# Performance work log

Hardware: AMD Instinct MI355X
Metric: run time of the kernel (lower is better)

Reference implementation:

```python
import jax, jax.numpy as jnp
import numpy as np
import math

H = 16          # num_attention_heads
D = 64          # attention_head_size
MAX_POS = 1024  # max_position_embeddings


def setup_inputs() -> dict:
    key = jax.random.key(0)
    ks = jax.random.split(key, 6)
    B, S, HID = 4, 1024, 1024
    scale = 1.0 / math.sqrt(HID)
    return {
        "hidden_states": jax.random.normal(ks[0], (B, S, HID), jnp.float32),
        "attention_mask": jnp.zeros((B, 1, 1, S), jnp.float32),
        "Wq": jax.random.normal(ks[1], (HID, HID), jnp.float32) * scale,
        "bq": jnp.zeros((HID,), jnp.float32),
        "Wk": jax.random.normal(ks[2], (HID, HID), jnp.float32) * scale,
        "bk": jnp.zeros((HID,), jnp.float32),
        "Wv": jax.random.normal(ks[3], (HID, HID), jnp.float32) * scale,
        "bv": jnp.zeros((HID,), jnp.float32),
        "dist_emb": jax.random.normal(ks[4], (2 * MAX_POS - 1, D), jnp.float32) * 0.02,
    }


def _split_heads(x):
    # [B,S,H*D] -> [B,H,S,D]
    B, S, _ = x.shape
    return x.reshape(B, S, H, D).transpose(0, 2, 1, 3)


def reference(hidden_states, attention_mask, Wq, bq, Wk, bk, Wv, bv, dist_emb):
    B, S, _ = hidden_states.shape
    q = _split_heads(hidden_states @ Wq.T + bq)   # [B,H,S,D]
    k = _split_heads(hidden_states @ Wk.T + bk)
    v = _split_heads(hidden_states @ Wv.T + bv)

    scores = jnp.einsum("bhqd,bhkd->bhqk", q, k)  # [B,H,S,S]

    # relative_key_query positional bias
    pos_l = jnp.arange(S)[:, None]
    pos_r = jnp.arange(S)[None, :]
    distance = pos_l - pos_r + (MAX_POS - 1)      # [S,S] in [0, 2*MAX_POS-2]
    pos_emb = dist_emb[distance]                  # [S,S,D]
    rel_q = jnp.einsum("bhld,lrd->bhlr", q, pos_emb)
    rel_k = jnp.einsum("bhrd,lrd->bhlr", k, pos_emb)
    scores = (scores + rel_q + rel_k) / math.sqrt(D)

    scores = scores + attention_mask
    probs = jax.nn.softmax(scores, axis=-1)
    ctx = jnp.einsum("bhqk,bhkd->bhqd", probs, v)  # [B,H,S,D]
    ctx = ctx.transpose(0, 2, 1, 3).reshape(B, S, H * D)
    return ctx
```

## Files before the change

kernel.cpp:

```cpp
#include <hip/hip_runtime.h>
#include <hip/hip_bf16.h>

#define B_   4
#define S_   1024
#define HID_ 1024
#define H_   16
#define D_   64

typedef __attribute__((ext_vector_type(4))) float f32x4;
typedef __attribute__((ext_vector_type(8))) __bf16 bf16v8;
typedef __attribute__((ext_vector_type(8))) unsigned short u16x8;

#define MFMA16(a, b, c) __builtin_amdgcn_mfma_f32_16x16x32_bf16((a), (b), (c), 0, 0, 0)
#define GLOAD16(gp, lp)                                                              \
    __builtin_amdgcn_global_load_lds((const __attribute__((address_space(1))) void*)(gp), \
                                     (__attribute__((address_space(3))) void*)(lp), 16, 0, 0)

__device__ __forceinline__ unsigned short f2bs_hw(float f) {
    __bf16 h = (__bf16)f;
    return __builtin_bit_cast(unsigned short, h);
}
__device__ __forceinline__ unsigned pack2bf(float a, float b) {
    unsigned short lo = f2bs_hw(a), hi = f2bs_hw(b);
    return (unsigned)lo | ((unsigned)hi << 16);
}
__device__ __forceinline__ float bs2f(unsigned short s) {
    union { unsigned u; float f; } v; v.u = ((unsigned)s) << 16;
    return v.f;
}

__global__ void conv_kernel(const float* __restrict__ src, unsigned short* __restrict__ dst,
                            int n4) {
    int i = blockIdx.x * 256 + threadIdx.x;
    if (i < n4) {
        float4 x = *(const float4*)(src + (size_t)i * 4);
        uint2 o;
        o.x = pack2bf(x.x, x.y);
        o.y = pack2bf(x.z, x.w);
        *(uint2*)(dst + (size_t)i * 4) = o;
    }
}

__global__ void conv4_kernel(const float* __restrict__ Wq, const float* __restrict__ Wk,
                             const float* __restrict__ Wv, const float* __restrict__ E,
                             unsigned short* __restrict__ Wqb, unsigned short* __restrict__ Wkb,
                             unsigned short* __restrict__ Wvb, unsigned short* __restrict__ Eb) {
    int bid = blockIdx.x;
    const float* src;
    unsigned short* dst;
    int n4, base;
    if (bid < 1024)      { src = Wq; dst = Wqb; n4 = 262144; base = bid; }
    else if (bid < 2048) { src = Wk; dst = Wkb; n4 = 262144; base = bid - 1024; }
    else if (bid < 3072) { src = Wv; dst = Wvb; n4 = 262144; base = bid - 2048; }
    else                 { src = E;  dst = Eb;  n4 = 32752;  base = bid - 3072; }
    int i = base * 256 + threadIdx.x;
    if (i < n4) {
        float4 x = *(const float4*)(src + (size_t)i * 4);
        uint2 o;
        o.x = pack2bf(x.x, x.y);
        o.y = pack2bf(x.z, x.w);
        *(uint2*)(dst + (size_t)i * 4) = o;
    }
}

__global__ __launch_bounds__(256)
void proj_kernel(const unsigned short* __restrict__ Xb,
                 const unsigned short* __restrict__ Wqb, const float* __restrict__ bq,
                 const unsigned short* __restrict__ Wkb, const float* __restrict__ bk,
                 const unsigned short* __restrict__ Wvb, const float* __restrict__ bv,
                 unsigned short* __restrict__ Qo, unsigned short* __restrict__ Ko,
                 unsigned short* __restrict__ Vo)
{
    __shared__ __align__(16) unsigned short Al[2][128][64];
    __shared__ __align__(16) unsigned short Bl[2][128][64];

    const int bid = blockIdx.x;
    const int tile = (bid & 7) * 96 + (bid >> 3);
    const int rt = tile / 24, ct = tile % 24;
    const int row0 = rt * 128, col0 = ct * 128;
    const int which = col0 >> 10;
    const unsigned short* Wm = (which == 0) ? Wqb : (which == 1) ? Wkb : Wvb;
    const float* bias        = (which == 0) ? bq  : (which == 1) ? bk  : bv;
    unsigned short* Out      = (which == 0) ? Qo  : (which == 1) ? Ko  : Vo;
    const int oc0 = col0 & 1023;

    const int t = threadIdx.x;
    const int lane = t & 63, w = t >> 6;
    const int wr = w >> 1, wc = w & 1;
    const int lg = lane >> 4, lc = lane & 15;

    f32x4 acc[4][4] = {};

#pragma unroll
    for (int l = 0; l < 4; ++l) {
        int idx = l * 256 + t;
        int r = idx >> 3, su = idx & 7;
        int u = su ^ (r & 7);
        GLOAD16(Xb + (size_t)(row0 + r) * 1024 + u * 8,
                &Al[0][0][0] + (size_t)(l * 256 + w * 64) * 8);
        GLOAD16(Wm + (size_t)(oc0 + r) * 1024 + u * 8,
                &Bl[0][0][0] + (size_t)(l * 256 + w * 64) * 8);
    }

    for (int it = 0; it < 16; ++it) {
        const int p = it & 1;
        __syncthreads();
        if (it < 15) {
            const int k1 = (it + 1) * 64;
#pragma unroll
            for (int l = 0; l < 4; ++l) {
                int idx = l * 256 + t;
                int r = idx >> 3, su = idx & 7;
                int u = su ^ (r & 7);
                GLOAD16(Xb + (size_t)(row0 + r) * 1024 + k1 + u * 8,
                        &Al[p ^ 1][0][0] + (size_t)(l * 256 + w * 64) * 8);
                GLOAD16(Wm + (size_t)(oc0 + r) * 1024 + k1 + u * 8,
                        &Bl[p ^ 1][0][0] + (size_t)(l * 256 + w * 64) * 8);
            }
        }
        bf16v8 af[4][2], bfg[4][2];
#pragma unroll
        for (int m = 0; m < 4; ++m)
#pragma unroll
            for (int ks = 0; ks < 2; ++ks) {
                int u = (ks * 4 + lg) ^ (lc & 7);
                af[m][ks] = *(const bf16v8*)&Al[p][wr * 64 + m * 16 + lc][u * 8];
            }
#pragma unroll
        for (int n = 0; n < 4; ++n)
#pragma unroll
            for (int ks = 0; ks < 2; ++ks) {
                int u = (ks * 4 + lg) ^ (lc & 7);
                bfg[n][ks] = *(const bf16v8*)&Bl[p][wc * 64 + n * 16 + lc][u * 8];
            }
        __builtin_amdgcn_s_setprio(1);
#pragma unroll
        for (int m = 0; m < 4; ++m)
#pragma unroll
            for (int n = 0; n < 4; ++n) {
                acc[m][n] = MFMA16(af[m][0], bfg[n][0], acc[m][n]);
                acc[m][n] = MFMA16(af[m][1], bfg[n][1], acc[m][n]);
            }
        __builtin_amdgcn_s_setprio(0);
    }

#pragma unroll
    for (int m = 0; m < 4; ++m)
#pragma unroll
        for (int n = 0; n < 4; ++n) {
            int j = oc0 + wc * 64 + n * 16 + lc;
            int hh = j >> 6, dd = j & 63;
            float bv_ = bias[j];
#pragma unroll
            for (int r = 0; r < 4; ++r) {
                int i = row0 + wr * 64 + m * 16 + lg * 4 + r;
                int bb = i >> 10, ss = i & 1023;
                float v = acc[m][n][r] + bv_;
                Out[((size_t)(bb * 16 + hh) * 1024 + ss) * 64 + dd] = f2bs_hw(v);
            }
        }
}

__global__ __launch_bounds__(256)
void attn_kernel(const unsigned short* __restrict__ Q,
                 const unsigned short* __restrict__ K,
                 const unsigned short* __restrict__ V,
                 const float* __restrict__ mask,
                 const unsigned short* __restrict__ Eb,
                 float* __restrict__ Out)
{
    __shared__ __align__(16) unsigned short Kl[64][64];
    __shared__ __align__(16) unsigned short El[128][64];
    __shared__ __align__(16) unsigned short VTl[64][72];
    __shared__ __align__(16) unsigned short QDl[64][134];
    __shared__ __align__(16) unsigned short KDl[64][134];
    __shared__ __align__(16) unsigned Pex[4 * 16 * 36];
    __shared__ float maskl[64];

    const int t = threadIdx.x;
    const int lane = t & 63, w = t >> 6;
    const int lg = lane >> 4, lc = lane & 15;

    const int bid = blockIdx.x;
    const int bh = bid & 63;
    const int qt = bid >> 6;
    const int b = bh >> 4, h = bh & 15;
    const int i0 = qt * 64;
    const int i_loc = w * 16 + lc;

    const float C2 = 0.125f * 1.44269504089f;
    const float L2E = 1.44269504089f;

    const unsigned short* Qh = Q + (size_t)bh * S_ * D_;
    const unsigned short* Kh = K + (size_t)bh * S_ * D_;
    const unsigned short* Vh = V + (size_t)bh * S_ * D_;

    bf16v8 qf[2];
#pragma unroll
    for (int ks = 0; ks < 2; ++ks)
        qf[ks] = *(const bf16v8*)(Qh + (size_t)(i0 + i_loc) * D_ + ks * 32 + lg * 8);

    u16x8 ones_u;
#pragma unroll
    for (int e = 0; e < 8; ++e) ones_u[e] = 0x3F80;
    const bf16v8 onesf = __builtin_bit_cast(bf16v8, ones_u);

    float m_r = -1e30f;
    f32x4 lacc = (f32x4){0.f, 0.f, 0.f, 0.f};
    f32x4 ctx[4];
#pragma unroll
    for (int nd = 0; nd < 4; ++nd) ctx[nd] = (f32x4){0.f, 0.f, 0.f, 0.f};

    unsigned* PexW = &Pex[(w * 16 + lc) * 36];

    const unsigned short* KD0 = &KDl[0][0] + lg * 4 * 133 + i_loc + 63;
    const unsigned short* QD0 = &QDl[0][0] + i_loc * 135 + 12 - lg * 4;

    const int va = t & 7, vrb = (t >> 3) << 1;
    const int vcq = va * 8;
    const int vjst = (vrb + (va << 3)) & 63;

    u16x8 v0c, v1c;
    float mkc;
    {
#pragma unroll
        for (int l = 0; l < 2; ++l) {
            int idx = l * 256 + t;
            int r = idx >> 3, su = idx & 7;
            int u = su ^ (r & 7);
            GLOAD16(Kh + (size_t)r * 64 + u * 8,
                    &Kl[0][0] + (size_t)(l * 256 + w * 64) * 8);
        }
        const int db0 = i0 + 960;
        const int sb0 = db0 & 127;
#pragma unroll
        for (int l = 0; l < 4; ++l) {
            int idx = l * 256 + t;
            int sl = idx >> 3, su = idx & 7;
            int u = su ^ (sl & 7);
            int dr = db0 + ((sl - sb0) & 127);
            if (dr > 2046) dr = 2046;
            GLOAD16(Eb + (size_t)dr * 64 + u * 8,
                    &El[0][0] + (size_t)(l * 256 + w * 64) * 8);
        }
        v0c = *(const u16x8*)(Vh + (size_t)vrb * 64 + vcq);
        v1c = *(const u16x8*)(Vh + (size_t)(vrb + 1) * 64 + vcq);
        mkc = (t < 64) ? mask[(size_t)b * S_ + t] * L2E : 0.f;
    }

    for (int jt = 0; jt < 16; ++jt) {
        const int j0 = jt * 64;
        const int dbase = i0 - j0 + 960;

        __syncthreads();
#pragma unroll
        for (int e = 0; e < 8; ++e)
            *(unsigned*)&VTl[vcq + e][vjst] = (unsigned)v0c[e] | ((unsigned)v1c[e] << 16);
        if (t < 64) maskl[t] = mkc;
        __syncthreads();

        bf16v8 kfa[2];
#pragma unroll
        for (int ks = 0; ks < 2; ++ks) {
            int u = (ks * 4 + lg) ^ (lc & 7);
            kfa[ks] = *(const bf16v8*)&Kl[w * 16 + lc][u * 8];
        }
        const int slb = dbase + lc;
        __builtin_amdgcn_s_setprio(1);
#pragma unroll
        for (int nd = 0; nd < 8; ++nd) {
            int sl = (slb + nd * 16) & 127;
            int u0 = lg ^ (lc & 7);
            int u1 = (4 + lg) ^ (lc & 7);
            bf16v8 ef0 = *(const bf16v8*)&El[sl][u0 * 8];
            bf16v8 ef1 = *(const bf16v8*)&El[sl][u1 * 8];
            f32x4 kd = (f32x4){0.f, 0.f, 0.f, 0.f};
            kd = MFMA16(ef0, kfa[0], kd);
            kd = MFMA16(ef1, kfa[1], kd);
            uint2 pk;
            pk.x = pack2bf(kd[0], kd[1]);
            pk.y = pack2bf(kd[2], kd[3]);
            *(uint2*)&KDl[w * 16 + lc][nd * 16 + lg * 4] = pk;
            f32x4 qd = (f32x4){0.f, 0.f, 0.f, 0.f};
            qd = MFMA16(ef0, qf[0], qd);
            qd = MFMA16(ef1, qf[1], qd);
            uint2 qk2;
            qk2.x = pack2bf(qd[0], qd[1]);
            qk2.y = pack2bf(qd[2], qd[3]);
            *(uint2*)&QDl[w * 16 + lc][nd * 16 + lg * 4] = qk2;
        }
        f32x4 s[4];
#pragma unroll
        for (int n = 0; n < 4; ++n) {
            s[n] = (f32x4){0.f, 0.f, 0.f, 0.f};
#pragma unroll
            for (int ks = 0; ks < 2; ++ks) {
                int u = (ks * 4 + lg) ^ (lc & 7);
                bf16v8 kb = *(const bf16v8*)&Kl[n * 16 + lc][u * 8];
                s[n] = MFMA16(kb, qf[ks], s[n]);
            }
        }
        __builtin_amdgcn_s_setprio(0);
        __syncthreads();

        if (jt < 15) {
            const int j0n = j0 + 64;
            const int dbn = dbase - 64;
            const int sbn = dbn & 127;
#pragma unroll
            for (int l = 0; l < 2; ++l) {
                int idx = l * 256 + t;
                int r = idx >> 3, su = idx & 7;
                int u = su ^ (r & 7);
                GLOAD16(Kh + (size_t)(j0n + r) * 64 + u * 8,
                        &Kl[0][0] + (size_t)(l * 256 + w * 64) * 8);
            }
#pragma unroll
            for (int l = 0; l < 2; ++l) {
                int idx = l * 256 + t;
                int rl = idx >> 3, su = idx & 7;
                int u = su ^ (rl & 7);
                GLOAD16(Eb + (size_t)(dbn + rl) * 64 + u * 8,
                        &El[sbn][0] + (size_t)(l * 256 + w * 64) * 8);
            }
            v0c = *(const u16x8*)(Vh + (size_t)(j0n + vrb) * 64 + vcq);
            v1c = *(const u16x8*)(Vh + (size_t)(j0n + vrb + 1) * 64 + vcq);
            mkc = (t < 64) ? mask[(size_t)b * S_ + j0n + t] * L2E : 0.f;
        }

        float vmax = -1e30f;
#pragma unroll
        for (int n = 0; n < 4; ++n) {
            float4 mk4 = *(const float4*)&maskl[n * 16 + lg * 4];
#pragma unroll
            for (int r = 0; r < 4; ++r) {
                float qdv = bs2f(QD0[51 - 16 * n - r]);
                float kdv = bs2f(KD0[133 * (16 * n + r)]);
                float mkr = (r == 0) ? mk4.x : (r == 1) ? mk4.y : (r == 2) ? mk4.z : mk4.w;
                float val = (s[n][r] + qdv + kdv) * C2 + mkr;
                s[n][r] = val;
                vmax = fmaxf(vmax, val);
            }
        }
        vmax = fmaxf(vmax, __shfl_xor(vmax, 16));
        vmax = fmaxf(vmax, __shfl_xor(vmax, 32));

        if (__any(vmax > m_r)) {
            float mnew = fmaxf(m_r, vmax);
            float alpha = exp2f(m_r - mnew);
            m_r = mnew;
#pragma unroll
            for (int r = 0; r < 4; ++r) lacc[r] *= alpha;
#pragma unroll
            for (int nd = 0; nd < 4; ++nd)
#pragma unroll
                for (int r = 0; r < 4; ++r)
                    ctx[nd][r] *= alpha;
        }

#pragma unroll
        for (int n = 0; n < 4; ++n)
#pragma unroll
            for (int r = 0; r < 4; ++r)
                s[n][r] = exp2f(s[n][r] - m_r);

#pragma unroll
        for (int n = 0; n < 4; ++n) {
            uint2 pk;
            pk.x = pack2bf(s[n][0], s[n][1]);
            pk.y = pack2bf(s[n][2], s[n][3]);
            *(uint2*)&PexW[n * 8 + lg * 2] = pk;
        }
        bf16v8 pfB[2];
#pragma unroll
        for (int ks = 0; ks < 2; ++ks) {
            int nc = 2 * ks + (lg >> 1);
            pfB[ks] = *(const bf16v8*)&PexW[nc * 8 + (lg & 1) * 4];
        }

        __builtin_amdgcn_s_setprio(1);
        lacc = MFMA16(onesf, pfB[0], lacc);
        lacc = MFMA16(onesf, pfB[1], lacc);
#pragma unroll
        for (int nd = 0; nd < 4; ++nd) {
            int vrow = nd * 16 + lc;
#pragma unroll
            for (int ks = 0; ks < 2; ++ks) {
                int jst = (ks * 32 + lg * 8 + ((vrow >> 3) << 3)) & 63;
                bf16v8 vf = *(const bf16v8*)&VTl[vrow][jst];
                ctx[nd] = MFMA16(vf, pfB[ks], ctx[nd]);
            }
        }
        __builtin_amdgcn_s_setprio(0);
    }

    float inv = 1.0f / lacc[0];
    float* outp = Out + ((size_t)(b * S_ + i0 + i_loc) * H_ + h) * D_;
#pragma unroll
    for (int nd = 0; nd < 4; ++nd) {
        float4 o;
        o.x = ctx[nd][0] * inv;
        o.y = ctx[nd][1] * inv;
        o.z = ctx[nd][2] * inv;
        o.w = ctx[nd][3] * inv;
        *(float4*)(outp + nd * 16 + lg * 4) = o;
    }
}

extern "C" void kernel_launch(void* const* d_in, const int* in_sizes, int n_in,
                              void* d_out, int out_size, void* d_ws, size_t ws_size,
                              hipStream_t stream)
{
    const float* X    = (const float*)d_in[0];
    const float* mask = (const float*)d_in[1];
    const float* Wq   = (const float*)d_in[2];
    const float* bq   = (const float*)d_in[3];
    const float* Wk   = (const float*)d_in[4];
    const float* bk   = (const float*)d_in[5];
    const float* Wv   = (const float*)d_in[6];
    const float* bv   = (const float*)d_in[7];
    const float* E    = (const float*)d_in[8];
    float* Out = (float*)d_out;

    const size_t headN = (size_t)B_ * H_ * S_ * D_;
    unsigned short* Qw  = (unsigned short*)d_ws;
    unsigned short* Kw  = Qw + headN;
    unsigned short* Vw  = Kw + headN;
    unsigned short* Ebw = Vw + headN;
    unsigned short* Xb  = Ebw + (size_t)2047 * 64;
    unsigned short* Wqb = Xb + (size_t)4096 * 1024;
    unsigned short* Wkb = Wqb + (size_t)1024 * 1024;
    unsigned short* Wvb = Wkb + (size_t)1024 * 1024;

    conv_kernel<<<dim3(4096), dim3(256), 0, stream>>>(X, Xb, 4096 * 1024 / 4);
    conv4_kernel<<<dim3(3200), dim3(256), 0, stream>>>(Wq, Wk, Wv, E, Wqb, Wkb, Wvb, Ebw);
    proj_kernel<<<dim3(768), dim3(256), 0, stream>>>(Xb, Wqb, bq, Wkb, bk, Wvb, bv, Qw, Kw, Vw);
    attn_kernel<<<dim3(1024), dim3(256), 0, stream>>>(Qw, Kw, Vw, mask, Ebw, Out);
}
```

Measured before the change: 173.5 us.

## Compute only needed diagonal band of rel-pos terms and drop register prefetch

Each wave now computes only the 5 diagonal-band 16-row tiles of the query-distance and key-distance products it needs, instead of all 8. Results are scattered straight into diagonal-aligned LDS buffers so they can be read back as vectors, and the mask is folded into the key-distance term. The register prefetch of the next K/E/V tiles is replaced by loading the current tile at the top of each iteration, which removes a barrier but loses the overlap of loads with compute. LDS use shrinks, and the Pex exchange buffer now aliases the QD buffer.

```diff
diff --git a/kernel.cpp b/kernel.cpp
--- a/kernel.cpp
+++ b/kernel.cpp
@@ -10,6 +10,7 @@
 typedef __attribute__((ext_vector_type(4))) float f32x4;
 typedef __attribute__((ext_vector_type(8))) __bf16 bf16v8;
 typedef __attribute__((ext_vector_type(8))) unsigned short u16x8;
+typedef __attribute__((ext_vector_type(4))) unsigned short u16x4;
 
 #define MFMA16(a, b, c) __builtin_amdgcn_mfma_f32_16x16x32_bf16((a), (b), (c), 0, 0, 0)
 #define GLOAD16(gp, lp)                                                              \
@@ -169,13 +170,11 @@
                  const unsigned short* __restrict__ Eb,
                  float* __restrict__ Out)
 {
+    __shared__ __align__(16) unsigned short El[128][64];
+    __shared__ __align__(16) unsigned short QDb[64][88];
+    __shared__ __align__(16) unsigned short VTl[64][72];
+    __shared__ __align__(16) unsigned short KDb[65][68];
     __shared__ __align__(16) unsigned short Kl[64][64];
-    __shared__ __align__(16) unsigned short El[128][64];
-    __shared__ __align__(16) unsigned short VTl[64][72];
-    __shared__ __align__(16) unsigned short QDl[64][134];
-    __shared__ __align__(16) unsigned short KDl[64][134];
-    __shared__ __align__(16) unsigned Pex[4 * 16 * 36];
-    __shared__ float maskl[64];
 
     const int t = threadIdx.x;
     const int lane = t & 63, w = t >> 6;
@@ -189,11 +188,11 @@
     const int i_loc = w * 16 + lc;
 
     const float C2 = 0.125f * 1.44269504089f;
-    const float L2E = 1.44269504089f;
 
     const unsigned short* Qh = Q + (size_t)bh * S_ * D_;
     const unsigned short* Kh = K + (size_t)bh * S_ * D_;
     const unsigned short* Vh = V + (size_t)bh * S_ * D_;
+    const float* maskb = mask + (size_t)b * S_ + w * 16 + lc;
 
     bf16v8 qf[2];
 #pragma unroll
@@ -211,133 +210,121 @@
 #pragma unroll
     for (int nd = 0; nd < 4; ++nd) ctx[nd] = (f32x4){0.f, 0.f, 0.f, 0.f};
 
-    unsigned* PexW = &Pex[(w * 16 + lc) * 36];
-
-    const unsigned short* KD0 = &KDl[0][0] + lg * 4 * 133 + i_loc + 63;
-    const unsigned short* QD0 = &QDl[0][0] + i_loc * 135 + 12 - lg * 4;
+    unsigned short* QDrow = &QDb[i_loc][0];
+    unsigned* PexW = (unsigned*)QDrow;
+    const int keyE = lc & 7;
 
     const int va = t & 7, vrb = (t >> 3) << 1;
     const int vcq = va * 8;
     const int vjst = (vrb + (va << 3)) & 63;
 
-    u16x8 v0c, v1c;
-    float mkc;
-    {
+    for (int jt = 0; jt < 16; ++jt) {
+        const int j0 = jt * 64;
+        const int dbase = i0 - j0 + 960;
+        __syncthreads();
+
 #pragma unroll
         for (int l = 0; l < 2; ++l) {
             int idx = l * 256 + t;
             int r = idx >> 3, su = idx & 7;
             int u = su ^ (r & 7);
-            GLOAD16(Kh + (size_t)r * 64 + u * 8,
+            GLOAD16(Kh + (size_t)(j0 + r) * 64 + u * 8,
                     &Kl[0][0] + (size_t)(l * 256 + w * 64) * 8);
         }
-        const int db0 = i0 + 960;
-        const int sb0 = db0 & 127;
-#pragma unroll
-        for (int l = 0; l < 4; ++l) {
-            int idx = l * 256 + t;
-            int sl = idx >> 3, su = idx & 7;
-            int u = su ^ (sl & 7);
-            int dr = db0 + ((sl - sb0) & 127);
-            if (dr > 2046) dr = 2046;
-            GLOAD16(Eb + (size_t)dr * 64 + u * 8,
-                    &El[0][0] + (size_t)(l * 256 + w * 64) * 8);
-        }
-        v0c = *(const u16x8*)(Vh + (size_t)vrb * 64 + vcq);
-        v1c = *(const u16x8*)(Vh + (size_t)(vrb + 1) * 64 + vcq);
-        mkc = (t < 64) ? mask[(size_t)b * S_ + t] * L2E : 0.f;
-    }
-
-    for (int jt = 0; jt < 16; ++jt) {
-        const int j0 = jt * 64;
-        const int dbase = i0 - j0 + 960;
-
-        __syncthreads();
-#pragma unroll
-        for (int e = 0; e < 8; ++e)
-            *(unsigned*)&VTl[vcq + e][vjst] = (unsigned)v0c[e] | ((unsigned)v1c[e] << 16);
-        if (t < 64) maskl[t] = mkc;
-        __syncthreads();
-
-        bf16v8 kfa[2];
-#pragma unroll
-        for (int ks = 0; ks < 2; ++ks) {
-            int u = (ks * 4 + lg) ^ (lc & 7);
-            kfa[ks] = *(const bf16v8*)&Kl[w * 16 + lc][u * 8];
-        }
-        const int slb = dbase + lc;
-        __builtin_amdgcn_s_setprio(1);
-#pragma unroll
-        for (int nd = 0; nd < 8; ++nd) {
-            int sl = (slb + nd * 16) & 127;
-            int u0 = lg ^ (lc & 7);
-            int u1 = (4 + lg) ^ (lc & 7);
-            bf16v8 ef0 = *(const bf16v8*)&El[sl][u0 * 8];
-            bf16v8 ef1 = *(const bf16v8*)&El[sl][u1 * 8];
-            f32x4 kd = (f32x4){0.f, 0.f, 0.f, 0.f};
-            kd = MFMA16(ef0, kfa[0], kd);
-            kd = MFMA16(ef1, kfa[1], kd);
-            uint2 pk;
-            pk.x = pack2bf(kd[0], kd[1]);
-            pk.y = pack2bf(kd[2], kd[3]);
-            *(uint2*)&KDl[w * 16 + lc][nd * 16 + lg * 4] = pk;
-            f32x4 qd = (f32x4){0.f, 0.f, 0.f, 0.f};
-            qd = MFMA16(ef0, qf[0], qd);
-            qd = MFMA16(ef1, qf[1], qd);
-            uint2 qk2;
-            qk2.x = pack2bf(qd[0], qd[1]);
-            qk2.y = pack2bf(qd[2], qd[3]);
-            *(uint2*)&QDl[w * 16 + lc][nd * 16 + lg * 4] = qk2;
-        }
-        f32x4 s[4];
-#pragma unroll
-        for (int n = 0; n < 4; ++n) {
-            s[n] = (f32x4){0.f, 0.f, 0.f, 0.f};
-#pragma unroll
-            for (int ks = 0; ks < 2; ++ks) {
-                int u = (ks * 4 + lg) ^ (lc & 7);
-                bf16v8 kb = *(const bf16v8*)&Kl[n * 16 + lc][u * 8];
-                s[n] = MFMA16(kb, qf[ks], s[n]);
-            }
-        }
-        __builtin_amdgcn_s_setprio(0);
-        __syncthreads();
-
-        if (jt < 15) {
-            const int j0n = j0 + 64;
-            const int dbn = dbase - 64;
-            const int sbn = dbn & 127;
-#pragma unroll
-            for (int l = 0; l < 2; ++l) {
+        {
+            u16x8 v0 = *(const u16x8*)(Vh + (size_t)(j0 + vrb) * 64 + vcq);
+            u16x8 v1 = *(const u16x8*)(Vh + (size_t)(j0 + vrb + 1) * 64 + vcq);
+#pragma unroll
+            for (int e = 0; e < 8; ++e)
+                *(unsigned*)&VTl[vcq + e][vjst] = (unsigned)v0[e] | ((unsigned)v1[e] << 16);
+        }
+        if (jt == 0) {
+            const int sb0 = dbase & 127;
+#pragma unroll
+            for (int l = 0; l < 4; ++l) {
                 int idx = l * 256 + t;
-                int r = idx >> 3, su = idx & 7;
-                int u = su ^ (r & 7);
-                GLOAD16(Kh + (size_t)(j0n + r) * 64 + u * 8,
-                        &Kl[0][0] + (size_t)(l * 256 + w * 64) * 8);
-            }
+                int sl = idx >> 3, su = idx & 7;
+                int u = su ^ (sl & 7);
+                int dr = dbase + ((sl - sb0) & 127);
+                if (dr > 2046) dr = 2046;
+                GLOAD16(Eb + (size_t)dr * 64 + u * 8,
+                        &El[0][0] + (size_t)(l * 256 + w * 64) * 8);
+            }
+        } else {
+            const int sb = dbase & 127;
 #pragma unroll
             for (int l = 0; l < 2; ++l) {
                 int idx = l * 256 + t;
                 int rl = idx >> 3, su = idx & 7;
                 int u = su ^ (rl & 7);
-                GLOAD16(Eb + (size_t)(dbn + rl) * 64 + u * 8,
-                        &El[sbn][0] + (size_t)(l * 256 + w * 64) * 8);
-            }
-            v0c = *(const u16x8*)(Vh + (size_t)(j0n + vrb) * 64 + vcq);
-            v1c = *(const u16x8*)(Vh + (size_t)(j0n + vrb + 1) * 64 + vcq);
-            mkc = (t < 64) ? mask[(size_t)b * S_ + j0n + t] * L2E : 0.f;
-        }
-
+                GLOAD16(Eb + (size_t)(dbase + rl) * 64 + u * 8,
+                        &El[sb][0] + (size_t)(l * 256 + w * 64) * 8);
+            }
+        }
+        float mk8 = 8.0f * maskb[j0];
+        __syncthreads();
+
+        bf16v8 kfa[2];
+#pragma unroll
+        for (int ks = 0; ks < 2; ++ks)
+            kfa[ks] = *(const bf16v8*)&Kl[w * 16 + lc][((ks * 4 + lg) ^ keyE) * 8];
+
+        __builtin_amdgcn_s_setprio(1);
+#pragma unroll
+        for (int ni = 0; ni < 5; ++ni) {
+            int sl = (dbase + w * 16 + ni * 16 + lc) & 127;
+            bf16v8 ef0 = *(const bf16v8*)&El[sl][(lg ^ keyE) * 8];
+            bf16v8 ef1 = *(const bf16v8*)&El[sl][((4 + lg) ^ keyE) * 8];
+            f32x4 qd = (f32x4){0.f, 0.f, 0.f, 0.f};
+            qd = MFMA16(ef0, qf[0], qd);
+            qd = MFMA16(ef1, qf[1], qd);
+            int slot0 = ni * 16 + 4 * lg - lc + 8;
+#pragma unroll
+            for (int r = 0; r < 4; ++r) {
+                int sw = slot0 + r;
+                sw = sw < 0 ? 0 : sw;
+                QDrow[sw] = f2bs_hw(qd[r]);
+            }
+        }
+#pragma unroll
+        for (int ni = 0; ni < 5; ++ni) {
+            int sl = (dbase + 48 - w * 16 + ni * 16 + lc) & 127;
+            bf16v8 ef0 = *(const bf16v8*)&El[sl][(lg ^ keyE) * 8];
+            bf16v8 ef1 = *(const bf16v8*)&El[sl][((4 + lg) ^ keyE) * 8];
+            f32x4 kd = (f32x4){0.f, 0.f, 0.f, 0.f};
+            kd = MFMA16(ef0, kfa[0], kd);
+            kd = MFMA16(ef1, kfa[1], kd);
+            int ib = ni * 16 + 4 * lg + lc - 15;
+#pragma unroll
+            for (int r = 0; r < 4; ++r) {
+                unsigned iw = (unsigned)(ib + r);
+                int row = (iw <= 63u) ? (int)iw : 64;
+                KDb[row][w * 16 + lc] = f2bs_hw(kd[r] + mk8);
+            }
+        }
+        f32x4 s[4];
+#pragma unroll
+        for (int n = 0; n < 4; ++n) {
+            s[n] = (f32x4){0.f, 0.f, 0.f, 0.f};
+#pragma unroll
+            for (int ks = 0; ks < 2; ++ks) {
+                bf16v8 kb = *(const bf16v8*)&Kl[n * 16 + lc][((ks * 4 + lg) ^ keyE) * 8];
+                s[n] = MFMA16(kb, qf[ks], s[n]);
+            }
+        }
+        __builtin_amdgcn_s_setprio(0);
+        __syncthreads();
+
+        const unsigned short* QDg = QDrow + 20 - 4 * lg;
+        const unsigned short* KDg = &KDb[i_loc][4 * lg];
         float vmax = -1e30f;
 #pragma unroll
         for (int n = 0; n < 4; ++n) {
-            float4 mk4 = *(const float4*)&maskl[n * 16 + lg * 4];
+            u16x4 qd4 = *(const u16x4*)(QDg + 48 - 16 * n);
+            u16x4 kd4 = *(const u16x4*)(KDg + 16 * n);
 #pragma unroll
             for (int r = 0; r < 4; ++r) {
-                float qdv = bs2f(QD0[51 - 16 * n - r]);
-                float kdv = bs2f(KD0[133 * (16 * n + r)]);
-                float mkr = (r == 0) ? mk4.x : (r == 1) ? mk4.y : (r == 2) ? mk4.z : mk4.w;
-                float val = (s[n][r] + qdv + kdv) * C2 + mkr;
+                float val = (s[n][r] + bs2f(qd4[3 - r]) + bs2f(kd4[r])) * C2;
                 s[n][r] = val;
                 vmax = fmaxf(vmax, val);
             }
```

Result: faster. 167.0 us (-3.7%).

## Reuse Q-distance products across key tiles and merge conversion kernels

Applied to the files above, without the earlier changes.

The query-by-distance-embedding product only shifts by one tile of distances for each key tile. It is now kept in a per-wave circular buffer indexed modulo 128, so after the first tile only half of the QD MFMAs are recomputed, and the shared-memory layouts and read indexing are changed to match. The separate X and weight bf16 conversion kernels are also merged into one launch. This trades extra modular index arithmetic and a correctness dependence on the ring-buffer slot mapping for fewer MFMAs and one fewer kernel launch.

```diff
diff --git a/kernel.cpp b/kernel.cpp
--- a/kernel.cpp
+++ b/kernel.cpp
@@ -10,6 +10,7 @@
 typedef __attribute__((ext_vector_type(4))) float f32x4;
 typedef __attribute__((ext_vector_type(8))) __bf16 bf16v8;
 typedef __attribute__((ext_vector_type(8))) unsigned short u16x8;
+typedef __attribute__((ext_vector_type(4))) unsigned short u16x4;
 
 #define MFMA16(a, b, c) __builtin_amdgcn_mfma_f32_16x16x32_bf16((a), (b), (c), 0, 0, 0)
 #define GLOAD16(gp, lp)                                                              \
@@ -29,30 +30,21 @@
     return v.f;
 }
 
-__global__ void conv_kernel(const float* __restrict__ src, unsigned short* __restrict__ dst,
-                            int n4) {
-    int i = blockIdx.x * 256 + threadIdx.x;
-    if (i < n4) {
-        float4 x = *(const float4*)(src + (size_t)i * 4);
-        uint2 o;
-        o.x = pack2bf(x.x, x.y);
-        o.y = pack2bf(x.z, x.w);
-        *(uint2*)(dst + (size_t)i * 4) = o;
-    }
-}
-
-__global__ void conv4_kernel(const float* __restrict__ Wq, const float* __restrict__ Wk,
-                             const float* __restrict__ Wv, const float* __restrict__ E,
-                             unsigned short* __restrict__ Wqb, unsigned short* __restrict__ Wkb,
-                             unsigned short* __restrict__ Wvb, unsigned short* __restrict__ Eb) {
+__global__ void convall_kernel(const float* __restrict__ X,
+                               const float* __restrict__ Wq, const float* __restrict__ Wk,
+                               const float* __restrict__ Wv, const float* __restrict__ E,
+                               unsigned short* __restrict__ Xb,
+                               unsigned short* __restrict__ Wqb, unsigned short* __restrict__ Wkb,
+                               unsigned short* __restrict__ Wvb, unsigned short* __restrict__ Eb) {
     int bid = blockIdx.x;
     const float* src;
     unsigned short* dst;
     int n4, base;
-    if (bid < 1024)      { src = Wq; dst = Wqb; n4 = 262144; base = bid; }
-    else if (bid < 2048) { src = Wk; dst = Wkb; n4 = 262144; base = bid - 1024; }
-    else if (bid < 3072) { src = Wv; dst = Wvb; n4 = 262144; base = bid - 2048; }
-    else                 { src = E;  dst = Eb;  n4 = 32752;  base = bid - 3072; }
+    if (bid < 4096)      { src = X;  dst = Xb;  n4 = 1048576; base = bid; }
+    else if (bid < 5120) { src = Wq; dst = Wqb; n4 = 262144;  base = bid - 4096; }
+    else if (bid < 6144) { src = Wk; dst = Wkb; n4 = 262144;  base = bid - 5120; }
+    else if (bid < 7168) { src = Wv; dst = Wvb; n4 = 262144;  base = bid - 6144; }
+    else                 { src = E;  dst = Eb;  n4 = 32752;   base = bid - 7168; }
     int i = base * 256 + threadIdx.x;
     if (i < n4) {
         float4 x = *(const float4*)(src + (size_t)i * 4);
@@ -172,8 +164,8 @@
     __shared__ __align__(16) unsigned short Kl[64][64];
     __shared__ __align__(16) unsigned short El[128][64];
     __shared__ __align__(16) unsigned short VTl[64][72];
-    __shared__ __align__(16) unsigned short QDl[64][134];
-    __shared__ __align__(16) unsigned short KDl[64][134];
+    __shared__ __align__(16) unsigned short QDl[4][16][136];
+    __shared__ __align__(16) unsigned short KDl[64][132];
     __shared__ __align__(16) unsigned Pex[4 * 16 * 36];
     __shared__ float maskl[64];
 
@@ -212,9 +204,6 @@
     for (int nd = 0; nd < 4; ++nd) ctx[nd] = (f32x4){0.f, 0.f, 0.f, 0.f};
 
     unsigned* PexW = &Pex[(w * 16 + lc) * 36];
-
-    const unsigned short* KD0 = &KDl[0][0] + lg * 4 * 133 + i_loc + 63;
-    const unsigned short* QD0 = &QDl[0][0] + i_loc * 135 + 12 - lg * 4;
 
     const int va = t & 7, vrb = (t >> 3) << 1;
     const int vcq = va * 8;
@@ -251,8 +240,8 @@
     for (int jt = 0; jt < 16; ++jt) {
         const int j0 = jt * 64;
         const int dbase = i0 - j0 + 960;
-
         __syncthreads();
+
 #pragma unroll
         for (int e = 0; e < 8; ++e)
             *(unsigned*)&VTl[vcq + e][vjst] = (unsigned)v0c[e] | ((unsigned)v1c[e] << 16);
@@ -265,11 +254,10 @@
             int u = (ks * 4 + lg) ^ (lc & 7);
             kfa[ks] = *(const bf16v8*)&Kl[w * 16 + lc][u * 8];
         }
-        const int slb = dbase + lc;
         __builtin_amdgcn_s_setprio(1);
 #pragma unroll
         for (int nd = 0; nd < 8; ++nd) {
-            int sl = (slb + nd * 16) & 127;
+            int sl = (dbase + nd * 16 + lc) & 127;
             int u0 = lg ^ (lc & 7);
             int u1 = (4 + lg) ^ (lc & 7);
             bf16v8 ef0 = *(const bf16v8*)&El[sl][u0 * 8];
@@ -281,13 +269,16 @@
             pk.x = pack2bf(kd[0], kd[1]);
             pk.y = pack2bf(kd[2], kd[3]);
             *(uint2*)&KDl[w * 16 + lc][nd * 16 + lg * 4] = pk;
-            f32x4 qd = (f32x4){0.f, 0.f, 0.f, 0.f};
-            qd = MFMA16(ef0, qf[0], qd);
-            qd = MFMA16(ef1, qf[1], qd);
-            uint2 qk2;
-            qk2.x = pack2bf(qd[0], qd[1]);
-            qk2.y = pack2bf(qd[2], qd[3]);
-            *(uint2*)&QDl[w * 16 + lc][nd * 16 + lg * 4] = qk2;
+            if (nd < 4 || jt == 0) {
+                f32x4 qd = (f32x4){0.f, 0.f, 0.f, 0.f};
+                qd = MFMA16(ef0, qf[0], qd);
+                qd = MFMA16(ef1, qf[1], qd);
+                int slot0 = ((dbase & 127) + nd * 16 + lg * 4) & 127;
+                uint2 qk2;
+                qk2.x = pack2bf(qd[0], qd[1]);
+                qk2.y = pack2bf(qd[2], qd[3]);
+                *(uint2*)&QDl[w][lc][slot0] = qk2;
+            }
         }
         f32x4 s[4];
 #pragma unroll
@@ -328,15 +319,19 @@
             mkc = (t < 64) ? mask[(size_t)b * S_ + j0n + t] * L2E : 0.f;
         }
 
+        const unsigned short* QDw = &QDl[w][lc][0];
         float vmax = -1e30f;
 #pragma unroll
         for (int n = 0; n < 4; ++n) {
-            float4 mk4 = *(const float4*)&maskl[n * 16 + lg * 4];
+            int jb = n * 16 + lg * 4;
+            float4 mk = *(const float4*)&maskl[jb];
+            int kbase = jb * 131 + i_loc + 63;
+            int qbase = dbase + i_loc - jb + 63;
 #pragma unroll
             for (int r = 0; r < 4; ++r) {
-                float qdv = bs2f(QD0[51 - 16 * n - r]);
-                float kdv = bs2f(KD0[133 * (16 * n + r)]);
-                float mkr = (r == 0) ? mk4.x : (r == 1) ? mk4.y : (r == 2) ? mk4.z : mk4.w;
+                float qdv = bs2f(QDw[(qbase - r) & 127]);
+                float kdv = bs2f((&KDl[0][0])[kbase + 131 * r]);
+                float mkr = (r == 0) ? mk.x : (r == 1) ? mk.y : (r == 2) ? mk.z : mk.w;
                 float val = (s[n][r] + qdv + kdv) * C2 + mkr;
                 s[n][r] = val;
                 vmax = fmaxf(vmax, val);
@@ -432,8 +427,8 @@
     unsigned short* Wkb = Wqb + (size_t)1024 * 1024;
     unsigned short* Wvb = Wkb + (size_t)1024 * 1024;
 
-    conv_kernel<<<dim3(4096), dim3(256), 0, stream>>>(X, Xb, 4096 * 1024 / 4);
-    conv4_kernel<<<dim3(3200), dim3(256), 0, stream>>>(Wq, Wk, Wv, E, Wqb, Wkb, Wvb, Ebw);
+    convall_kernel<<<dim3(7296), dim3(256), 0, stream>>>(X, Wq, Wk, Wv, E,
+                                                         Xb, Wqb, Wkb, Wvb, Ebw);
     proj_kernel<<<dim3(768), dim3(256), 0, stream>>>(Xb, Wqb, bq, Wkb, bk, Wvb, bv, Qw, Kw, Vw);
     attn_kernel<<<dim3(1024), dim3(256), 0, stream>>>(Qw, Kw, Vw, mask, Ebw, Out);
 }
```

Measured after the change: 149.3 us. 13.9% less time.
